# Kernel optimization log

Measured on AMD Instinct MI355X. Metric: run time of the kernel, lower is better.

The kernel has to match this reference:

```python
import jax, jax.numpy as jnp
import numpy as np
import math

HIDDEN = 768
HEADS = 12
HEAD_DIM = HIDDEN // HEADS  # 64
SEQ = 197
K_RANK = min(128, HEAD_DIM)  # 64
BATCH = 64


def setup_inputs() -> dict:
    key = jax.random.key(0)
    ks = jax.random.split(key, 12)
    init = 0.02
    # Linear weights stored [in, out] (equivalent to torch W.T)
    return {
        "hidden_states": jax.random.normal(ks[0], (BATCH, SEQ, HIDDEN), dtype=jnp.float32),
        "Wq": jax.random.normal(ks[1], (HIDDEN, HIDDEN), dtype=jnp.float32) * init,
        "bq": jnp.zeros((HIDDEN,), dtype=jnp.float32),
        "Wk": jax.random.normal(ks[2], (HIDDEN, HIDDEN), dtype=jnp.float32) * init,
        "bk": jnp.zeros((HIDDEN,), dtype=jnp.float32),
        "Wv": jax.random.normal(ks[3], (HIDDEN, HIDDEN), dtype=jnp.float32) * init,
        "bv": jnp.zeros((HIDDEN,), dtype=jnp.float32),
        "Wo": jax.random.normal(ks[4], (HIDDEN, HIDDEN), dtype=jnp.float32) * init,
        "bo": jnp.zeros((HIDDEN,), dtype=jnp.float32),
        "E_k": jax.random.normal(ks[5], (SEQ, K_RANK), dtype=jnp.float32) * init,
        "E_v": jax.random.normal(ks[6], (SEQ, K_RANK), dtype=jnp.float32) * init,
    }


def reference(hidden_states, Wq, bq, Wk, bk, Wv, bv, Wo, bo, E_k, E_v):
    B, S, D = hidden_states.shape
    H, d = HEADS, HEAD_DIM
    scale = 1.0 / math.sqrt(d)

    def split_heads(x):  # [B,S,D] -> [B,H,S,d]
        return x.reshape(B, S, H, d).transpose(0, 2, 1, 3)

    q = split_heads(hidden_states @ Wq + bq)
    k = split_heads(hidden_states @ Wk + bk)
    v = split_heads(hidden_states @ Wv + bv)

    # low-rank projection of K/V along the sequence axis: [B,H,k,d]
    pk = jnp.einsum('sk,bhsd->bhkd', E_k, k)
    pv = jnp.einsum('sk,bhsd->bhkd', E_v, v)

    # scores over reduced axis: [B,H,S,k]
    scores = jnp.einsum('bhsd,bhkd->bhsk', q, pk) * scale
    probs = jax.nn.softmax(scores, axis=-1)

    ctx = jnp.einsum('bhsk,bhkd->bhsd', probs, pv)
    ctx = ctx.transpose(0, 2, 1, 3).reshape(B, S, D)
    out = ctx @ Wo + bo  # dropout rate 0.0 -> identity
    return out
```

## Files before the change

### kernel.cpp

```cpp
#include <hip/hip_runtime.h>
#include <math.h>

#define B_   64
#define S_   197
#define D_   768
#define H_   12
#define HD_  64
#define M_   (B_ * S_)
#define MPAD 12672
#define KE   224
#define BH_  (B_ * H_)
#define WSZ  ((size_t)D_ * D_)

typedef _Float16 half8_t __attribute__((ext_vector_type(8)));
typedef _Float16 half4_t __attribute__((ext_vector_type(4)));
typedef _Float16 half2_t __attribute__((ext_vector_type(2)));
typedef float floatx4 __attribute__((ext_vector_type(4)));

#define LDS_DMA16(gptr, lptr) \
  __builtin_amdgcn_global_load_lds((const __attribute__((address_space(1))) void*)(gptr), \
                                   (__attribute__((address_space(3))) void*)(lptr), 16, 0, 0)

__global__ __launch_bounds__(256) void prep_y_kernel(
    const float* __restrict__ X,
    const float* __restrict__ Wq, const float* __restrict__ Wk,
    const float* __restrict__ Wv, const float* __restrict__ Wo,
    const float* __restrict__ Ek, const float* __restrict__ Ev,
    _Float16* __restrict__ Xh,
    _Float16* __restrict__ Tcat, _Float16* __restrict__ To,
    float* __restrict__ esumK, float* __restrict__ esumV,
    _Float16* __restrict__ Ybuf)
{
    __shared__ _Float16 smem[KE * 66];
    const int bid = blockIdx.x, tid = threadIdx.x;

    int task, idx;
    if (bid < 9984) {
        const int q = bid / 13, r = bid - q * 13;
        if (r == 0) { task = 0; idx = q; }
        else        { task = 1; idx = 12 * q + r - 1; }
    } else if (bid < 10272) { task = 1; idx = 9216 + (bid - 9984); }
    else if (bid < 12576)   { task = 2; idx = bid - 10272; }
    else                    { task = 3; idx = bid - 12576; }

    if (task == 1) {
        const int i4 = (idx * 256 + tid) * 4;
        float4 v = make_float4(0.f, 0.f, 0.f, 0.f);
        if (i4 < M_ * D_) v = *(const float4*)&X[i4];
        half4_t o = { (_Float16)v.x, (_Float16)v.y, (_Float16)v.z, (_Float16)v.w };
        *(half4_t*)&Xh[i4] = o;
        return;
    }

    if (task == 2) {
        float (*tile)[33] = (float (*)[33])smem;
        const int z = idx / 576, rem = idx % 576;
        const int bx = rem % 24, by = rem / 24;
        const float* W = (z == 0) ? Wk : (z == 1) ? Wv : (z == 2) ? Wq : Wo;
        _Float16* T = (z < 3) ? (Tcat + (size_t)z * WSZ) : To;
        const int n0 = bx * 32, k0 = by * 32;
        const int r = tid >> 3, c4 = (tid & 7) * 4;
        *(float4*)&tile[r][c4] = *(const float4*)&W[(size_t)(k0 + r) * D_ + n0 + c4];
        __syncthreads();
        half4_t o = { (_Float16)tile[c4 + 0][r], (_Float16)tile[c4 + 1][r],
                      (_Float16)tile[c4 + 2][r], (_Float16)tile[c4 + 3][r] };
        *(half4_t*)&T[(size_t)(n0 + r) * D_ + k0 + c4] = o;
        return;
    }

    if (task == 3) {
        const float* E = idx ? Ev : Ek;
        float* es = idx ? esumV : esumK;
        if (tid < 64) {
            float acc = 0.f;
            for (int s = 0; s < S_; ++s) acc += E[s * 64 + tid];
            es[tid] = acc;
        }
        return;
    }

    _Float16* Xs = smem;
    const int b = idx / 12, n0 = (idx % 12) * 64;
    const int w = tid >> 6, lane = tid & 63;
    const int l15 = lane & 15, quad = lane >> 4;

    #pragma unroll
    for (int i = 0; i < 7; ++i) {
        const int s = i * 32 + (tid >> 3);
        const int d0 = (tid & 7) * 8;
        float4 v0 = make_float4(0.f, 0.f, 0.f, 0.f), v1 = v0;
        if (s < S_) {
            const float* src = &X[(size_t)(b * S_ + s) * D_ + n0 + d0];
            v0 = *(const float4*)src;
            v1 = *(const float4*)(src + 4);
        }
        const _Float16 h[8] = { (_Float16)v0.x, (_Float16)v0.y, (_Float16)v0.z,
                                (_Float16)v0.w, (_Float16)v1.x, (_Float16)v1.y,
                                (_Float16)v1.z, (_Float16)v1.w };
        #pragma unroll
        for (int jj = 0; jj < 4; ++jj) {
            half2_t t2 = { h[2 * jj], h[2 * jj + 1] };
            *(half2_t*)&Xs[s * 66 + d0 + 2 * jj] = t2;
        }
    }
    __syncthreads();

    floatx4 acc[2][4] = {};
    #pragma unroll
    for (int k7 = 0; k7 < 7; ++k7) {
        half8_t af[2];
        #pragma unroll
        for (int mi = 0; mi < 2; ++mi) {
            const int row = w * 32 + mi * 16 + l15;
            const float* Esrc = (row < 64) ? Ek : Ev;
            const int er = row & 63;
            #pragma unroll
            for (int jj = 0; jj < 8; ++jj) {
                const int s = k7 * 32 + quad * 8 + jj;
                af[mi][jj] = (_Float16)((s < S_) ? Esrc[s * 64 + er] : 0.f);
            }
        }
        #pragma unroll
        for (int ni = 0; ni < 4; ++ni) {
            const int sb = k7 * 32 + quad * 8;
            half8_t bf;
            #pragma unroll
            for (int jj = 0; jj < 8; ++jj) bf[jj] = Xs[(sb + jj) * 66 + ni * 16 + l15];
            #pragma unroll
            for (int mi = 0; mi < 2; ++mi)
                acc[mi][ni] = __builtin_amdgcn_mfma_f32_16x16x32_f16(
                    af[mi], bf, acc[mi][ni], 0, 0, 0);
        }
    }

    #pragma unroll
    for (int mi = 0; mi < 2; ++mi)
        #pragma unroll
        for (int ni = 0; ni < 4; ++ni)
            #pragma unroll
            for (int i = 0; i < 4; ++i) {
                const int m_local = w * 32 + mi * 16 + quad * 4 + i;
                const int row = (m_local >> 6) * 4096 + b * 64 + (m_local & 63);
                Ybuf[(size_t)row * D_ + n0 + ni * 16 + l15] = (_Float16)acc[mi][ni][i];
            }
}

__global__ __launch_bounds__(256) void gemm_qpkv(
    const _Float16* __restrict__ Xh, const _Float16* __restrict__ Ybuf,
    const _Float16* __restrict__ Tcat,
    const float* __restrict__ bq, const float* __restrict__ bk,
    const float* __restrict__ bv,
    const float* __restrict__ esumK, const float* __restrict__ esumV,
    _Float16* __restrict__ Qh, _Float16* __restrict__ pk16,
    _Float16* __restrict__ pv16)
{
    __shared__ _Float16 sm[32768];
    const int bid = blockIdx.x;
    const _Float16 *A, *W;
    const float *bias, *esum;
    _Float16* O16;
    int m0, n0, rowb;
    if (bid < 624) {
        const int xcd = bid & 7, t = bid >> 3;
        const int slot = t / 6, j = t - slot * 6;
        const int m_blk = slot * 8 + xcd;
        if (m_blk >= MPAD / 128) return;
        m0 = m_blk * 128; n0 = j * 128; rowb = m0;
        A = Xh; W = Tcat + 2 * WSZ + (size_t)n0 * D_;
        bias = bq; esum = nullptr; O16 = Qh;
    } else {
        const int b2 = bid - 624;
        const int xcd = b2 & 7, t = b2 >> 3;
        const int slot = t / 6, j = t - slot * 6;
        const int m_blk = slot * 8 + xcd;
        m0 = m_blk * 128; n0 = j * 128;
        const bool pv = (m_blk >= 32);
        rowb = pv ? m0 - 4096 : m0;
        A = Ybuf; W = Tcat + (pv ? WSZ : 0) + (size_t)n0 * D_;
        bias = pv ? bv : bk; esum = pv ? esumV : esumK;
        O16 = pv ? pv16 : pk16;
    }

    const int tid = threadIdx.x;
    const int w = tid >> 6, lane = tid & 63;
    const int fr = lane & 15, quad = lane >> 4, f7 = lane & 7;
    const int l3 = lane >> 3;
    const int csrc = ((lane & 7) ^ l3) * 8;
    const int wm = (w >> 1) * 64, wn = (w & 1) * 64;

    const _Float16* Abase = A + (size_t)(m0 + w * 32 + l3) * D_ + csrc;
    const _Float16* Wbase = W + (size_t)(w * 32 + l3) * D_ + csrc;

    floatx4 acc[4][4] = {};

#define QPKV_STAGE(BUF, K0) \
    { _Pragma("unroll") \
      for (int j = 0; j < 4; ++j) { \
          LDS_DMA16(Abase + (size_t)(j * 8) * D_ + (K0), &sm[(BUF) * 16384 + w * 2048 + j * 512]); \
          LDS_DMA16(Wbase + (size_t)(j * 8) * D_ + (K0), &sm[(BUF) * 16384 + 8192 + w * 2048 + j * 512]); \
      } }

#define QPKV_COMPUTE(BUF) \
    { _Pragma("unroll") \
      for (int ksub = 0; ksub < 2; ++ksub) { \
          const int sa = ((ksub * 4 + quad) ^ f7) * 8; \
          half8_t af[4], bf[4]; \
          _Pragma("unroll") \
          for (int i = 0; i < 4; ++i) { \
              af[i] = *(const half8_t*)&sm[(BUF) * 16384 + (wm + i * 16 + fr) * 64 + sa]; \
              bf[i] = *(const half8_t*)&sm[(BUF) * 16384 + 8192 + (wn + i * 16 + fr) * 64 + sa]; \
          } \
          _Pragma("unroll") \
          for (int mi = 0; mi < 4; ++mi) \
              _Pragma("unroll") \
              for (int ni = 0; ni < 4; ++ni) \
                  acc[mi][ni] = __builtin_amdgcn_mfma_f32_16x16x32_f16( \
                      af[mi], bf[ni], acc[mi][ni], 0, 0, 0); \
      } }

    QPKV_STAGE(0, 0);
    __syncthreads();
    #pragma unroll
    for (int t = 0; t < 10; t += 2) {
        QPKV_STAGE(1, (t + 1) * 64);
        QPKV_COMPUTE(0);
        __syncthreads();
        QPKV_STAGE(0, (t + 2) * 64);
        QPKV_COMPUTE(1);
        __syncthreads();
    }
    QPKV_STAGE(1, 11 * 64);
    QPKV_COMPUTE(0);
    __syncthreads();
    QPKV_COMPUTE(1);

    float bval[4];
    #pragma unroll
    for (int ni = 0; ni < 4; ++ni)
        bval[ni] = bias[n0 + wn + ni * 16 + fr];

    _Float16* ct = &sm[w * 2176];
    #pragma unroll
    for (int half = 0; half < 2; ++half) {
        #pragma unroll
        for (int mi2 = 0; mi2 < 2; ++mi2) {
            const int mi = half * 2 + mi2;
            float esv[4] = {1.f, 1.f, 1.f, 1.f};
            if (esum) {
                const float4 es4 = *(const float4*)&esum[mi * 16 + quad * 4];
                esv[0] = es4.x; esv[1] = es4.y; esv[2] = es4.z; esv[3] = es4.w;
            }
            #pragma unroll
            for (int ni = 0; ni < 4; ++ni)
                #pragma unroll
                for (int i = 0; i < 4; ++i)
                    ct[(mi2 * 16 + quad * 4 + i) * 68 + ni * 16 + fr] =
                        (_Float16)(acc[mi][ni][i] + esv[i] * bval[ni]);
        }
        #pragma unroll
        for (int pass = 0; pass < 4; ++pass) {
            const int rr = pass * 8 + (lane >> 3);
            const int cc = (lane & 7) * 8;
            const half8_t v = *(const half8_t*)&ct[rr * 68 + cc];
            *(half8_t*)&O16[(size_t)(rowb + wm + half * 32 + rr) * D_ + n0 + wn + cc] = v;
        }
    }
}

__global__ __launch_bounds__(256) void gemm_o(
    const _Float16* __restrict__ CTX, const _Float16* __restrict__ To,
    const float* __restrict__ bo, float* __restrict__ O32)
{
    __shared__ _Float16 sm[32768];
    const int xcd = blockIdx.x & 7, t = blockIdx.x >> 3;
    const int slot = t / 6, j = t - slot * 6;
    const int m_blk = slot * 8 + xcd;
    if (m_blk >= MPAD / 128) return;
    const int m0 = m_blk * 128, n0 = j * 128;

    const int tid = threadIdx.x;
    const int w = tid >> 6, lane = tid & 63;
    const int fr = lane & 15, quad = lane >> 4, f7 = lane & 7;
    const int l3 = lane >> 3;
    const int csrc = ((lane & 7) ^ l3) * 8;
    const int wm = (w >> 1) * 64, wn = (w & 1) * 64;

    const _Float16* Abase = CTX + (size_t)(m0 + w * 32 + l3) * D_ + csrc;
    const _Float16* Wbase = To + (size_t)(n0 + w * 32 + l3) * D_ + csrc;

    floatx4 acc[4][4] = {};

    QPKV_STAGE(0, 0);
    __syncthreads();
    #pragma unroll
    for (int t2 = 0; t2 < 10; t2 += 2) {
        QPKV_STAGE(1, (t2 + 1) * 64);
        QPKV_COMPUTE(0);
        __syncthreads();
        QPKV_STAGE(0, (t2 + 2) * 64);
        QPKV_COMPUTE(1);
        __syncthreads();
    }
    QPKV_STAGE(1, 11 * 64);
    QPKV_COMPUTE(0);
    __syncthreads();
    QPKV_COMPUTE(1);

    float bval[4];
    #pragma unroll
    for (int ni = 0; ni < 4; ++ni)
        bval[ni] = bo[n0 + wn + ni * 16 + fr];

    const bool full = (m0 + 128 <= M_);
    #pragma unroll
    for (int ni = 0; ni < 4; ++ni) {
        const int n = n0 + wn + ni * 16 + fr;
        #pragma unroll
        for (int mi = 0; mi < 4; ++mi)
            #pragma unroll
            for (int i = 0; i < 4; ++i) {
                const int m = m0 + wm + mi * 16 + quad * 4 + i;
                if (full || m < M_)
                    O32[(size_t)m * D_ + n] = acc[mi][ni][i] + bval[ni];
            }
    }
}

__global__ __launch_bounds__(256) void attn_kernel(
    const _Float16* __restrict__ Qh, const _Float16* __restrict__ pk16,
    const _Float16* __restrict__ pv16, _Float16* __restrict__ CTXh)
{
    __shared__ _Float16 P[64 * 80];
    const int bh = blockIdx.x, b = bh / H_, h = bh % H_;
    const int tid = threadIdx.x, w = tid >> 6, lane = tid & 63;
    const int l15 = lane & 15, quad = lane >> 4;
    const _Float16* pkB = pk16 + (size_t)(b * 64) * D_ + h * 64;
    const _Float16* pvB = pv16 + (size_t)(b * 64) * D_ + h * 64;
    const size_t qbase = (size_t)(b * S_) * D_ + h * HD_;

    half8_t bkf[4][2], bvf[4][2];
    #pragma unroll
    for (int ni = 0; ni < 4; ++ni)
        #pragma unroll
        for (int kk = 0; kk < 2; ++kk) {
            bkf[ni][kk] = *(const half8_t*)&pkB[(size_t)(ni * 16 + l15) * D_ + kk * 32 + quad * 8];
            #pragma unroll
            for (int jj = 0; jj < 8; ++jj)
                bvf[ni][kk][jj] = pvB[(size_t)(kk * 32 + quad * 8 + jj) * D_ + ni * 16 + l15];
        }

    for (int t = w; t < 13; t += 4) {
        const int srow = t * 16;
        floatx4 acc[4] = {};
        #pragma unroll
        for (int kk = 0; kk < 2; ++kk) {
            const half8_t aq = *(const half8_t*)
                &Qh[qbase + (size_t)(srow + l15) * D_ + kk * 32 + quad * 8];
            #pragma unroll
            for (int ni = 0; ni < 4; ++ni)
                acc[ni] = __builtin_amdgcn_mfma_f32_16x16x32_f16(
                    aq, bkf[ni][kk], acc[ni], 0, 0, 0);
        }
        float p[4][4];
        #pragma unroll
        for (int i = 0; i < 4; ++i) {
            const float s0 = acc[0][i] * 0.125f, s1 = acc[1][i] * 0.125f;
            const float s2 = acc[2][i] * 0.125f, s3 = acc[3][i] * 0.125f;
            float mx = fmaxf(fmaxf(s0, s1), fmaxf(s2, s3));
            #pragma unroll
            for (int off = 1; off < 16; off <<= 1)
                mx = fmaxf(mx, __shfl_xor(mx, off, 64));
            const float e0 = __expf(s0 - mx), e1 = __expf(s1 - mx);
            const float e2 = __expf(s2 - mx), e3 = __expf(s3 - mx);
            float sme = e0 + e1 + e2 + e3;
            #pragma unroll
            for (int off = 1; off < 16; off <<= 1)
                sme += __shfl_xor(sme, off, 64);
            const float inv = 1.f / sme;
            p[0][i] = e0 * inv; p[1][i] = e1 * inv;
            p[2][i] = e2 * inv; p[3][i] = e3 * inv;
        }
        #pragma unroll
        for (int ni = 0; ni < 4; ++ni)
            #pragma unroll
            for (int i = 0; i < 4; ++i)
                P[(w * 16 + quad * 4 + i) * 80 + ni * 16 + l15] = (_Float16)p[ni][i];

        floatx4 accv[4] = {};
        #pragma unroll
        for (int kk = 0; kk < 2; ++kk) {
            const half8_t ap = *(const half8_t*)&P[(w * 16 + l15) * 80 + kk * 32 + quad * 8];
            #pragma unroll
            for (int ni = 0; ni < 4; ++ni)
                accv[ni] = __builtin_amdgcn_mfma_f32_16x16x32_f16(
                    ap, bvf[ni][kk], accv[ni], 0, 0, 0);
        }
        #pragma unroll
        for (int ni = 0; ni < 4; ++ni)
            #pragma unroll
            for (int i = 0; i < 4; ++i) {
                const int s = srow + quad * 4 + i;
                if (s < S_)
                    CTXh[qbase + (size_t)s * D_ + ni * 16 + l15] = (_Float16)accv[ni][i];
            }
    }
}

extern "C" void kernel_launch(void* const* d_in, const int* in_sizes, int n_in,
                              void* d_out, int out_size, void* d_ws, size_t ws_size,
                              hipStream_t stream) {
    const float* X   = (const float*)d_in[0];
    const float* Wq  = (const float*)d_in[1];
    const float* bq  = (const float*)d_in[2];
    const float* Wk  = (const float*)d_in[3];
    const float* bk  = (const float*)d_in[4];
    const float* Wv  = (const float*)d_in[5];
    const float* bv  = (const float*)d_in[6];
    const float* Wo  = (const float*)d_in[7];
    const float* bo  = (const float*)d_in[8];
    const float* E_k = (const float*)d_in[9];
    const float* E_v = (const float*)d_in[10];
    float* out = (float*)d_out;

    char* p = (char*)d_ws;
    _Float16* Xh   = (_Float16*)p; p += (size_t)MPAD * D_ * 2;
    _Float16* Tcat = (_Float16*)p; p += (size_t)3 * WSZ * 2;
    _Float16* To   = (_Float16*)p; p += (size_t)WSZ * 2;
    _Float16* Qh   = (_Float16*)p; p += (size_t)MPAD * D_ * 2;
    float* esumK   = (float*)p;    p += 64 * sizeof(float);
    float* esumV   = (float*)p;    p += 64 * sizeof(float);
    _Float16* Ybuf = (_Float16*)p; p += (size_t)8192 * D_ * 2;
    _Float16* pk16 = (_Float16*)p; p += (size_t)4096 * D_ * 2;
    _Float16* pv16 = (_Float16*)p;

    prep_y_kernel<<<12578, 256, 0, stream>>>(X, Wq, Wk, Wv, Wo, E_k, E_v,
                                             Xh, Tcat, To, esumK, esumV, Ybuf);
    gemm_qpkv<<<1008, 256, 0, stream>>>(Xh, Ybuf, Tcat,
                                        bq, bk, bv, esumK, esumV,
                                        Qh, pk16, pv16);
    attn_kernel<<<BH_, 256, 0, stream>>>(Qh, pk16, pv16, Xh);
    gemm_o<<<624, 256, 0, stream>>>(Xh, To, bo, out);
}
```

Before: 202.0 us.

## Fuse fp32-to-fp16 conversion of X into the Q projection GEMM A-load

Drops the separate pass that converts the whole hidden_states tensor to fp16 in the prep kernel. The Q GEMM now reads fp32 X directly into registers, converts it and writes it to LDS, replacing the async LDS DMA path for the A operand. This removes one full write and read of an fp16 copy of X. The cost is register-staged loads with bounds checks and reads of twice as many bytes per A tile, which may weaken load/compute overlap in the Q blocks.

```diff
diff --git a/kernel.cpp b/kernel.cpp
--- a/kernel.cpp
+++ b/kernel.cpp
@@ -26,7 +26,6 @@
     const float* __restrict__ Wq, const float* __restrict__ Wk,
     const float* __restrict__ Wv, const float* __restrict__ Wo,
     const float* __restrict__ Ek, const float* __restrict__ Ev,
-    _Float16* __restrict__ Xh,
     _Float16* __restrict__ Tcat, _Float16* __restrict__ To,
     float* __restrict__ esumK, float* __restrict__ esumV,
     _Float16* __restrict__ Ybuf)
@@ -34,25 +33,8 @@
     __shared__ _Float16 smem[KE * 66];
     const int bid = blockIdx.x, tid = threadIdx.x;
 
-    int task, idx;
-    if (bid < 9984) {
-        const int q = bid / 13, r = bid - q * 13;
-        if (r == 0) { task = 0; idx = q; }
-        else        { task = 1; idx = 12 * q + r - 1; }
-    } else if (bid < 10272) { task = 1; idx = 9216 + (bid - 9984); }
-    else if (bid < 12576)   { task = 2; idx = bid - 10272; }
-    else                    { task = 3; idx = bid - 12576; }
-
-    if (task == 1) {
-        const int i4 = (idx * 256 + tid) * 4;
-        float4 v = make_float4(0.f, 0.f, 0.f, 0.f);
-        if (i4 < M_ * D_) v = *(const float4*)&X[i4];
-        half4_t o = { (_Float16)v.x, (_Float16)v.y, (_Float16)v.z, (_Float16)v.w };
-        *(half4_t*)&Xh[i4] = o;
-        return;
-    }
-
-    if (task == 2) {
+    if (bid >= 768 && bid < 3072) {
+        const int idx = bid - 768;
         float (*tile)[33] = (float (*)[33])smem;
         const int z = idx / 576, rem = idx % 576;
         const int bx = rem % 24, by = rem / 24;
@@ -68,7 +50,8 @@
         return;
     }
 
-    if (task == 3) {
+    if (bid >= 3072) {
+        const int idx = bid - 3072;
         const float* E = idx ? Ev : Ek;
         float* es = idx ? esumV : esumK;
         if (tid < 64) {
@@ -80,6 +63,7 @@
     }
 
     _Float16* Xs = smem;
+    const int idx = bid;
     const int b = idx / 12, n0 = (idx % 12) * 64;
     const int w = tid >> 6, lane = tid & 63;
     const int l15 = lane & 15, quad = lane >> 4;
@@ -146,7 +130,7 @@
 }
 
 __global__ __launch_bounds__(256) void gemm_qpkv(
-    const _Float16* __restrict__ Xh, const _Float16* __restrict__ Ybuf,
+    const float* __restrict__ X, const _Float16* __restrict__ Ybuf,
     const _Float16* __restrict__ Tcat,
     const float* __restrict__ bq, const float* __restrict__ bk,
     const float* __restrict__ bv,
@@ -156,18 +140,19 @@
 {
     __shared__ _Float16 sm[32768];
     const int bid = blockIdx.x;
-    const _Float16 *A, *W;
+    const _Float16 *W;
     const float *bias, *esum;
     _Float16* O16;
     int m0, n0, rowb;
+    bool isQ;
     if (bid < 624) {
         const int xcd = bid & 7, t = bid >> 3;
         const int slot = t / 6, j = t - slot * 6;
         const int m_blk = slot * 8 + xcd;
         if (m_blk >= MPAD / 128) return;
         m0 = m_blk * 128; n0 = j * 128; rowb = m0;
-        A = Xh; W = Tcat + 2 * WSZ + (size_t)n0 * D_;
-        bias = bq; esum = nullptr; O16 = Qh;
+        W = Tcat + 2 * WSZ + (size_t)n0 * D_;
+        bias = bq; esum = nullptr; O16 = Qh; isQ = true;
     } else {
         const int b2 = bid - 624;
         const int xcd = b2 & 7, t = b2 >> 3;
@@ -176,9 +161,9 @@
         m0 = m_blk * 128; n0 = j * 128;
         const bool pv = (m_blk >= 32);
         rowb = pv ? m0 - 4096 : m0;
-        A = Ybuf; W = Tcat + (pv ? WSZ : 0) + (size_t)n0 * D_;
+        W = Tcat + (pv ? WSZ : 0) + (size_t)n0 * D_;
         bias = pv ? bv : bk; esum = pv ? esumV : esumK;
-        O16 = pv ? pv16 : pk16;
+        O16 = pv ? pv16 : pk16; isQ = false;
     }
 
     const int tid = threadIdx.x;
@@ -188,19 +173,15 @@
     const int csrc = ((lane & 7) ^ l3) * 8;
     const int wm = (w >> 1) * 64, wn = (w & 1) * 64;
 
-    const _Float16* Abase = A + (size_t)(m0 + w * 32 + l3) * D_ + csrc;
     const _Float16* Wbase = W + (size_t)(w * 32 + l3) * D_ + csrc;
-
     floatx4 acc[4][4] = {};
 
-#define QPKV_STAGE(BUF, K0) \
+#define STAGE_B(BUF, K0) \
     { _Pragma("unroll") \
-      for (int j = 0; j < 4; ++j) { \
-          LDS_DMA16(Abase + (size_t)(j * 8) * D_ + (K0), &sm[(BUF) * 16384 + w * 2048 + j * 512]); \
-          LDS_DMA16(Wbase + (size_t)(j * 8) * D_ + (K0), &sm[(BUF) * 16384 + 8192 + w * 2048 + j * 512]); \
-      } }
-
-#define QPKV_COMPUTE(BUF) \
+      for (int j = 0; j < 4; ++j) \
+          LDS_DMA16(Wbase + (size_t)(j * 8) * D_ + (K0), &sm[(BUF) * 16384 + 8192 + w * 2048 + j * 512]); }
+
+#define COMPUTE(BUF) \
     { _Pragma("unroll") \
       for (int ksub = 0; ksub < 2; ++ksub) { \
           const int sa = ((ksub * 4 + quad) ^ f7) * 8; \
@@ -218,21 +199,73 @@
                       af[mi], bf[ni], acc[mi][ni], 0, 0, 0); \
       } }
 
-    QPKV_STAGE(0, 0);
-    __syncthreads();
-    #pragma unroll
-    for (int t = 0; t < 10; t += 2) {
-        QPKV_STAGE(1, (t + 1) * 64);
-        QPKV_COMPUTE(0);
-        __syncthreads();
-        QPKV_STAGE(0, (t + 2) * 64);
-        QPKV_COMPUTE(1);
-        __syncthreads();
-    }
-    QPKV_STAGE(1, 11 * 64);
-    QPKV_COMPUTE(0);
-    __syncthreads();
-    QPKV_COMPUTE(1);
+    if (isQ) {
+        const float* Xbase = X + (size_t)(m0 + w * 32 + l3) * D_ + csrc;
+        float4 ra[4][2];
+        const float4 z4 = make_float4(0.f, 0.f, 0.f, 0.f);
+
+#define LOADA(K0) \
+        { _Pragma("unroll") \
+          for (int j = 0; j < 4; ++j) { \
+              const int r = m0 + w * 32 + j * 8 + l3; \
+              if (r < M_) { \
+                  ra[j][0] = *(const float4*)(Xbase + (size_t)(j * 8) * D_ + (K0)); \
+                  ra[j][1] = *(const float4*)(Xbase + (size_t)(j * 8) * D_ + (K0) + 4); \
+              } else { ra[j][0] = z4; ra[j][1] = z4; } \
+          } }
+
+#define WRITE_A(BUF) \
+        { _Pragma("unroll") \
+          for (int j = 0; j < 4; ++j) { \
+              half8_t o = { (_Float16)ra[j][0].x, (_Float16)ra[j][0].y, \
+                            (_Float16)ra[j][0].z, (_Float16)ra[j][0].w, \
+                            (_Float16)ra[j][1].x, (_Float16)ra[j][1].y, \
+                            (_Float16)ra[j][1].z, (_Float16)ra[j][1].w }; \
+              *(half8_t*)&sm[(BUF) * 16384 + w * 2048 + j * 512 + lane * 8] = o; \
+          } }
+
+        LOADA(0); STAGE_B(0, 0); WRITE_A(0);
+        __syncthreads();
+        #pragma unroll
+        for (int t = 0; t < 10; t += 2) {
+            LOADA((t + 1) * 64); STAGE_B(1, (t + 1) * 64);
+            COMPUTE(0);
+            WRITE_A(1);
+            __syncthreads();
+            LOADA((t + 2) * 64); STAGE_B(0, (t + 2) * 64);
+            COMPUTE(1);
+            WRITE_A(0);
+            __syncthreads();
+        }
+        LOADA(11 * 64); STAGE_B(1, 11 * 64);
+        COMPUTE(0);
+        WRITE_A(1);
+        __syncthreads();
+        COMPUTE(1);
+    } else {
+        const _Float16* Abase = Ybuf + (size_t)(m0 + w * 32 + l3) * D_ + csrc;
+
+#define STAGE_A16(BUF, K0) \
+        { _Pragma("unroll") \
+          for (int j = 0; j < 4; ++j) \
+              LDS_DMA16(Abase + (size_t)(j * 8) * D_ + (K0), &sm[(BUF) * 16384 + w * 2048 + j * 512]); }
+
+        STAGE_A16(0, 0); STAGE_B(0, 0);
+        __syncthreads();
+        #pragma unroll
+        for (int t = 0; t < 10; t += 2) {
+            STAGE_A16(1, (t + 1) * 64); STAGE_B(1, (t + 1) * 64);
+            COMPUTE(0);
+            __syncthreads();
+            STAGE_A16(0, (t + 2) * 64); STAGE_B(0, (t + 2) * 64);
+            COMPUTE(1);
+            __syncthreads();
+        }
+        STAGE_A16(1, 11 * 64); STAGE_B(1, 11 * 64);
+        COMPUTE(0);
+        __syncthreads();
+        COMPUTE(1);
+    }
 
     float bval[4];
     #pragma unroll
@@ -290,21 +323,28 @@
 
     floatx4 acc[4][4] = {};
 
-    QPKV_STAGE(0, 0);
+#define O_STAGE(BUF, K0) \
+    { _Pragma("unroll") \
+      for (int j2 = 0; j2 < 4; ++j2) { \
+          LDS_DMA16(Abase + (size_t)(j2 * 8) * D_ + (K0), &sm[(BUF) * 16384 + w * 2048 + j2 * 512]); \
+          LDS_DMA16(Wbase + (size_t)(j2 * 8) * D_ + (K0), &sm[(BUF) * 16384 + 8192 + w * 2048 + j2 * 512]); \
+      } }
+
+    O_STAGE(0, 0);
     __syncthreads();
     #pragma unroll
     for (int t2 = 0; t2 < 10; t2 += 2) {
-        QPKV_STAGE(1, (t2 + 1) * 64);
-        QPKV_COMPUTE(0);
-        __syncthreads();
-        QPKV_STAGE(0, (t2 + 2) * 64);
-        QPKV_COMPUTE(1);
-        __syncthreads();
-    }
-    QPKV_STAGE(1, 11 * 64);
-    QPKV_COMPUTE(0);
+        O_STAGE(1, (t2 + 1) * 64);
+        COMPUTE(0);
+        __syncthreads();
+        O_STAGE(0, (t2 + 2) * 64);
+        COMPUTE(1);
+        __syncthreads();
+    }
+    O_STAGE(1, 11 * 64);
+    COMPUTE(0);
     __syncthreads();
-    QPKV_COMPUTE(1);
+    COMPUTE(1);
 
     float bval[4];
     #pragma unroll
@@ -423,7 +463,7 @@
     float* out = (float*)d_out;
 
     char* p = (char*)d_ws;
-    _Float16* Xh   = (_Float16*)p; p += (size_t)MPAD * D_ * 2;
+    _Float16* CTXh = (_Float16*)p; p += (size_t)MPAD * D_ * 2;
     _Float16* Tcat = (_Float16*)p; p += (size_t)3 * WSZ * 2;
     _Float16* To   = (_Float16*)p; p += (size_t)WSZ * 2;
     _Float16* Qh   = (_Float16*)p; p += (size_t)MPAD * D_ * 2;
@@ -433,11 +473,11 @@
     _Float16* pk16 = (_Float16*)p; p += (size_t)4096 * D_ * 2;
     _Float16* pv16 = (_Float16*)p;
 
-    prep_y_kernel<<<12578, 256, 0, stream>>>(X, Wq, Wk, Wv, Wo, E_k, E_v,
-                                             Xh, Tcat, To, esumK, esumV, Ybuf);
-    gemm_qpkv<<<1008, 256, 0, stream>>>(Xh, Ybuf, Tcat,
+    prep_y_kernel<<<3074, 256, 0, stream>>>(X, Wq, Wk, Wv, Wo, E_k, E_v,
+                                            Tcat, To, esumK, esumV, Ybuf);
+    gemm_qpkv<<<1008, 256, 0, stream>>>(X, Ybuf, Tcat,
                                         bq, bk, bv, esumK, esumV,
                                         Qh, pk16, pv16);
-    attn_kernel<<<BH_, 256, 0, stream>>>(Qh, pk16, pv16, Xh);
-    gemm_o<<<624, 256, 0, stream>>>(Xh, To, bo, out);
+    attn_kernel<<<BH_, 256, 0, stream>>>(Qh, pk16, pv16, CTXh);
+    gemm_o<<<624, 256, 0, stream>>>(CTXh, To, bo, out);
 }
```

After: 220.0 us. 1.09x slower.

## Fuse attention and output projection into a single kernel

Applied to the files above, without the earlier changes.

Replaces the separate attention kernel and the output-projection GEMM with one kernel. Each block handles 32 sequence rows of one batch across all 12 heads, one wave per 3 heads, and keeps the context tile in LDS. It then multiplies that tile by the Wo weights, read directly from global memory, and writes the fp32 output with bias. This removes the fp16 context round trip through global memory and one kernel launch. In exchange, Wo is re-read by every block with little register reuse and no LDS staging, and far fewer blocks run than the tiled GEMM used.

```diff
diff --git a/kernel.cpp b/kernel.cpp
--- a/kernel.cpp
+++ b/kernel.cpp
@@ -11,6 +11,7 @@
 #define KE   224
 #define BH_  (B_ * H_)
 #define WSZ  ((size_t)D_ * D_)
+#define CW   776
 
 typedef _Float16 half8_t __attribute__((ext_vector_type(8)));
 typedef _Float16 half4_t __attribute__((ext_vector_type(4)));
@@ -267,141 +268,142 @@
     }
 }
 
-__global__ __launch_bounds__(256) void gemm_o(
-    const _Float16* __restrict__ CTX, const _Float16* __restrict__ To,
+__global__ __launch_bounds__(256) void attn_o_kernel(
+    const _Float16* __restrict__ Qh, const _Float16* __restrict__ pk16,
+    const _Float16* __restrict__ pv16, const _Float16* __restrict__ To,
     const float* __restrict__ bo, float* __restrict__ O32)
 {
-    __shared__ _Float16 sm[32768];
-    const int xcd = blockIdx.x & 7, t = blockIdx.x >> 3;
-    const int slot = t / 6, j = t - slot * 6;
-    const int m_blk = slot * 8 + xcd;
-    if (m_blk >= MPAD / 128) return;
-    const int m0 = m_blk * 128, n0 = j * 128;
-
-    const int tid = threadIdx.x;
-    const int w = tid >> 6, lane = tid & 63;
-    const int fr = lane & 15, quad = lane >> 4, f7 = lane & 7;
-    const int l3 = lane >> 3;
-    const int csrc = ((lane & 7) ^ l3) * 8;
-    const int wm = (w >> 1) * 64, wn = (w & 1) * 64;
-
-    const _Float16* Abase = CTX + (size_t)(m0 + w * 32 + l3) * D_ + csrc;
-    const _Float16* Wbase = To + (size_t)(n0 + w * 32 + l3) * D_ + csrc;
-
-    floatx4 acc[4][4] = {};
-
-    QPKV_STAGE(0, 0);
-    __syncthreads();
-    #pragma unroll
-    for (int t2 = 0; t2 < 10; t2 += 2) {
-        QPKV_STAGE(1, (t2 + 1) * 64);
-        QPKV_COMPUTE(0);
-        __syncthreads();
-        QPKV_STAGE(0, (t2 + 2) * 64);
-        QPKV_COMPUTE(1);
-        __syncthreads();
-    }
-    QPKV_STAGE(1, 11 * 64);
-    QPKV_COMPUTE(0);
-    __syncthreads();
-    QPKV_COMPUTE(1);
-
-    float bval[4];
-    #pragma unroll
-    for (int ni = 0; ni < 4; ++ni)
-        bval[ni] = bo[n0 + wn + ni * 16 + fr];
-
-    const bool full = (m0 + 128 <= M_);
-    #pragma unroll
-    for (int ni = 0; ni < 4; ++ni) {
-        const int n = n0 + wn + ni * 16 + fr;
-        #pragma unroll
-        for (int mi = 0; mi < 4; ++mi)
-            #pragma unroll
-            for (int i = 0; i < 4; ++i) {
-                const int m = m0 + wm + mi * 16 + quad * 4 + i;
-                if (full || m < M_)
-                    O32[(size_t)m * D_ + n] = acc[mi][ni][i] + bval[ni];
-            }
-    }
-}
-
-__global__ __launch_bounds__(256) void attn_kernel(
-    const _Float16* __restrict__ Qh, const _Float16* __restrict__ pk16,
-    const _Float16* __restrict__ pv16, _Float16* __restrict__ CTXh)
-{
-    __shared__ _Float16 P[64 * 80];
-    const int bh = blockIdx.x, b = bh / H_, h = bh % H_;
+    __shared__ _Float16 ctx[32 * CW];
+    const int bid = blockIdx.x;
+    const int b = bid & 63, st = bid >> 6;
+    const int srow0 = st * 32;
     const int tid = threadIdx.x, w = tid >> 6, lane = tid & 63;
     const int l15 = lane & 15, quad = lane >> 4;
-    const _Float16* pkB = pk16 + (size_t)(b * 64) * D_ + h * 64;
-    const _Float16* pvB = pv16 + (size_t)(b * 64) * D_ + h * 64;
-    const size_t qbase = (size_t)(b * S_) * D_ + h * HD_;
-
-    half8_t bkf[4][2], bvf[4][2];
-    #pragma unroll
-    for (int ni = 0; ni < 4; ++ni)
+
+    _Float16* P = &ctx[(w * 3 + 2) * 64];
+
+    for (int hh = 0; hh < 3; ++hh) {
+        const int h = w * 3 + hh;
+        const _Float16* pkB = pk16 + (size_t)(b * 64) * D_ + h * 64;
+        const _Float16* pvB = pv16 + (size_t)(b * 64) * D_ + h * 64;
+        const size_t qbase = (size_t)(b * S_) * D_ + h * HD_;
+
+        half8_t bkf[4][2], bvf[4][2];
+        #pragma unroll
+        for (int ni = 0; ni < 4; ++ni)
+            #pragma unroll
+            for (int kk = 0; kk < 2; ++kk) {
+                bkf[ni][kk] = *(const half8_t*)&pkB[(size_t)(ni * 16 + l15) * D_ + kk * 32 + quad * 8];
+                #pragma unroll
+                for (int jj = 0; jj < 8; ++jj)
+                    bvf[ni][kk][jj] = pvB[(size_t)(kk * 32 + quad * 8 + jj) * D_ + ni * 16 + l15];
+            }
+
+        floatx4 acc[2][4] = {};
         #pragma unroll
         for (int kk = 0; kk < 2; ++kk) {
-            bkf[ni][kk] = *(const half8_t*)&pkB[(size_t)(ni * 16 + l15) * D_ + kk * 32 + quad * 8];
-            #pragma unroll
-            for (int jj = 0; jj < 8; ++jj)
-                bvf[ni][kk][jj] = pvB[(size_t)(kk * 32 + quad * 8 + jj) * D_ + ni * 16 + l15];
-        }
-
-    for (int t = w; t < 13; t += 4) {
-        const int srow = t * 16;
-        floatx4 acc[4] = {};
+            half8_t aq[2];
+            #pragma unroll
+            for (int mi = 0; mi < 2; ++mi)
+                aq[mi] = *(const half8_t*)
+                    &Qh[qbase + (size_t)(srow0 + mi * 16 + l15) * D_ + kk * 32 + quad * 8];
+            #pragma unroll
+            for (int ni = 0; ni < 4; ++ni)
+                #pragma unroll
+                for (int mi = 0; mi < 2; ++mi)
+                    acc[mi][ni] = __builtin_amdgcn_mfma_f32_16x16x32_f16(
+                        aq[mi], bkf[ni][kk], acc[mi][ni], 0, 0, 0);
+        }
+
+        #pragma unroll
+        for (int mi = 0; mi < 2; ++mi) {
+            float p[4][4];
+            #pragma unroll
+            for (int i = 0; i < 4; ++i) {
+                const float s0 = acc[mi][0][i] * 0.125f, s1 = acc[mi][1][i] * 0.125f;
+                const float s2 = acc[mi][2][i] * 0.125f, s3 = acc[mi][3][i] * 0.125f;
+                float mx = fmaxf(fmaxf(s0, s1), fmaxf(s2, s3));
+                #pragma unroll
+                for (int off = 1; off < 16; off <<= 1)
+                    mx = fmaxf(mx, __shfl_xor(mx, off, 64));
+                const float e0 = __expf(s0 - mx), e1 = __expf(s1 - mx);
+                const float e2 = __expf(s2 - mx), e3 = __expf(s3 - mx);
+                float sme = e0 + e1 + e2 + e3;
+                #pragma unroll
+                for (int off = 1; off < 16; off <<= 1)
+                    sme += __shfl_xor(sme, off, 64);
+                const float inv = 1.f / sme;
+                p[0][i] = e0 * inv; p[1][i] = e1 * inv;
+                p[2][i] = e2 * inv; p[3][i] = e3 * inv;
+            }
+            #pragma unroll
+            for (int ni = 0; ni < 4; ++ni)
+                #pragma unroll
+                for (int i = 0; i < 4; ++i)
+                    P[(mi * 16 + quad * 4 + i) * CW + ni * 16 + l15] = (_Float16)p[ni][i];
+        }
+
+        floatx4 accv[2][4] = {};
         #pragma unroll
         for (int kk = 0; kk < 2; ++kk) {
-            const half8_t aq = *(const half8_t*)
-                &Qh[qbase + (size_t)(srow + l15) * D_ + kk * 32 + quad * 8];
+            half8_t ap[2];
+            #pragma unroll
+            for (int mi = 0; mi < 2; ++mi)
+                ap[mi] = *(const half8_t*)&P[(mi * 16 + l15) * CW + kk * 32 + quad * 8];
             #pragma unroll
             for (int ni = 0; ni < 4; ++ni)
-                acc[ni] = __builtin_amdgcn_mfma_f32_16x16x32_f16(
-                    aq, bkf[ni][kk], acc[ni], 0, 0, 0);
-        }
-        float p[4][4];
-        #pragma unroll
-        for (int i = 0; i < 4; ++i) {
-            const float s0 = acc[0][i] * 0.125f, s1 = acc[1][i] * 0.125f;
-            const float s2 = acc[2][i] * 0.125f, s3 = acc[3][i] * 0.125f;
-            float mx = fmaxf(fmaxf(s0, s1), fmaxf(s2, s3));
-            #pragma unroll
-            for (int off = 1; off < 16; off <<= 1)
-                mx = fmaxf(mx, __shfl_xor(mx, off, 64));
-            const float e0 = __expf(s0 - mx), e1 = __expf(s1 - mx);
-            const float e2 = __expf(s2 - mx), e3 = __expf(s3 - mx);
-            float sme = e0 + e1 + e2 + e3;
-            #pragma unroll
-            for (int off = 1; off < 16; off <<= 1)
-                sme += __shfl_xor(sme, off, 64);
-            const float inv = 1.f / sme;
-            p[0][i] = e0 * inv; p[1][i] = e1 * inv;
-            p[2][i] = e2 * inv; p[3][i] = e3 * inv;
-        }
-        #pragma unroll
-        for (int ni = 0; ni < 4; ++ni)
-            #pragma unroll
-            for (int i = 0; i < 4; ++i)
-                P[(w * 16 + quad * 4 + i) * 80 + ni * 16 + l15] = (_Float16)p[ni][i];
-
-        floatx4 accv[4] = {};
-        #pragma unroll
-        for (int kk = 0; kk < 2; ++kk) {
-            const half8_t ap = *(const half8_t*)&P[(w * 16 + l15) * 80 + kk * 32 + quad * 8];
+                #pragma unroll
+                for (int mi = 0; mi < 2; ++mi)
+                    accv[mi][ni] = __builtin_amdgcn_mfma_f32_16x16x32_f16(
+                        ap[mi], bvf[ni][kk], accv[mi][ni], 0, 0, 0);
+        }
+        #pragma unroll
+        for (int mi = 0; mi < 2; ++mi)
             #pragma unroll
             for (int ni = 0; ni < 4; ++ni)
-                accv[ni] = __builtin_amdgcn_mfma_f32_16x16x32_f16(
-                    ap, bvf[ni][kk], accv[ni], 0, 0, 0);
-        }
-        #pragma unroll
-        for (int ni = 0; ni < 4; ++ni)
+                #pragma unroll
+                for (int i = 0; i < 4; ++i)
+                    ctx[(mi * 16 + quad * 4 + i) * CW + h * 64 + ni * 16 + l15] =
+                        (_Float16)accv[mi][ni][i];
+    }
+    __syncthreads();
+
+    float bval[12];
+    #pragma unroll
+    for (int nf = 0; nf < 12; ++nf)
+        bval[nf] = bo[w * 192 + nf * 16 + l15];
+
+    floatx4 oacc[2][12] = {};
+    for (int k0 = 0; k0 < 12; ++k0) {
+        #pragma unroll
+        for (int ksub = 0; ksub < 2; ++ksub) {
+            const int ka = k0 * 64 + ksub * 32 + quad * 8;
+            half8_t af[2];
+            #pragma unroll
+            for (int mi = 0; mi < 2; ++mi)
+                af[mi] = *(const half8_t*)&ctx[(mi * 16 + l15) * CW + ka];
+            #pragma unroll
+            for (int nf = 0; nf < 12; ++nf) {
+                const half8_t bf = *(const half8_t*)
+                    &To[(size_t)(w * 192 + nf * 16 + l15) * D_ + ka];
+                #pragma unroll
+                for (int mi = 0; mi < 2; ++mi)
+                    oacc[mi][nf] = __builtin_amdgcn_mfma_f32_16x16x32_f16(
+                        af[mi], bf, oacc[mi][nf], 0, 0, 0);
+            }
+        }
+    }
+
+    #pragma unroll
+    for (int nf = 0; nf < 12; ++nf) {
+        const int n = w * 192 + nf * 16 + l15;
+        #pragma unroll
+        for (int mi = 0; mi < 2; ++mi)
             #pragma unroll
             for (int i = 0; i < 4; ++i) {
-                const int s = srow + quad * 4 + i;
+                const int s = srow0 + mi * 16 + quad * 4 + i;
                 if (s < S_)
-                    CTXh[qbase + (size_t)s * D_ + ni * 16 + l15] = (_Float16)accv[ni][i];
+                    O32[(size_t)(b * S_ + s) * D_ + n] = oacc[mi][nf][i] + bval[nf];
             }
     }
 }
@@ -438,6 +440,5 @@
     gemm_qpkv<<<1008, 256, 0, stream>>>(Xh, Ybuf, Tcat,
                                         bq, bk, bv, esumK, esumV,
                                         Qh, pk16, pv16);
-    attn_kernel<<<BH_, 256, 0, stream>>>(Qh, pk16, pv16, Xh);
-    gemm_o<<<624, 256, 0, stream>>>(Xh, To, bo, out);
+    attn_o_kernel<<<448, 256, 0, stream>>>(Qh, pk16, pv16, To, bo, out);
 }
```

New measurement: 292.3 us. 44.7% more time.

## Fuse X fp16 conversion into Y-projection blocks and store projected V transposed

Applied to the files above, without the earlier changes.

The separate elementwise blocks that converted X to fp16 are removed; each Y-projection block already reads its X tile, so it now also writes the fp16 copy to Xh, and a few small blocks zero the padded tail rows. This avoids reading X from global memory twice and shrinks the prep grid. In addition, the projected V is written transposed ([D][4096]) through LDS in the GEMM epilogue, so the attention kernel can load V fragments with one 16-byte vector load instead of eight strided scalar loads. The cost is an extra LDS transpose pass in the GEMM epilogue.

```diff
diff --git a/kernel.cpp b/kernel.cpp
--- a/kernel.cpp
+++ b/kernel.cpp
@@ -34,25 +34,8 @@
     __shared__ _Float16 smem[KE * 66];
     const int bid = blockIdx.x, tid = threadIdx.x;
 
-    int task, idx;
-    if (bid < 9984) {
-        const int q = bid / 13, r = bid - q * 13;
-        if (r == 0) { task = 0; idx = q; }
-        else        { task = 1; idx = 12 * q + r - 1; }
-    } else if (bid < 10272) { task = 1; idx = 9216 + (bid - 9984); }
-    else if (bid < 12576)   { task = 2; idx = bid - 10272; }
-    else                    { task = 3; idx = bid - 12576; }
-
-    if (task == 1) {
-        const int i4 = (idx * 256 + tid) * 4;
-        float4 v = make_float4(0.f, 0.f, 0.f, 0.f);
-        if (i4 < M_ * D_) v = *(const float4*)&X[i4];
-        half4_t o = { (_Float16)v.x, (_Float16)v.y, (_Float16)v.z, (_Float16)v.w };
-        *(half4_t*)&Xh[i4] = o;
-        return;
-    }
-
-    if (task == 2) {
+    if (bid >= 768 && bid < 3072) {
+        const int idx = bid - 768;
         float (*tile)[33] = (float (*)[33])smem;
         const int z = idx / 576, rem = idx % 576;
         const int bx = rem % 24, by = rem / 24;
@@ -68,7 +51,8 @@
         return;
     }
 
-    if (task == 3) {
+    if (bid >= 3096) {
+        const int idx = bid - 3096;
         const float* E = idx ? Ev : Ek;
         float* es = idx ? esumV : esumK;
         if (tid < 64) {
@@ -79,7 +63,15 @@
         return;
     }
 
+    if (bid >= 3072) {
+        const int idx = bid - 3072;
+        const half8_t z8 = {};
+        *(half8_t*)&Xh[(size_t)M_ * D_ + (size_t)(idx * 256 + tid) * 8] = z8;
+        return;
+    }
+
     _Float16* Xs = smem;
+    const int idx = bid;
     const int b = idx / 12, n0 = (idx % 12) * 64;
     const int w = tid >> 6, lane = tid & 63;
     const int l15 = lane & 15, quad = lane >> 4;
@@ -94,12 +86,14 @@
             v0 = *(const float4*)src;
             v1 = *(const float4*)(src + 4);
         }
-        const _Float16 h[8] = { (_Float16)v0.x, (_Float16)v0.y, (_Float16)v0.z,
-                                (_Float16)v0.w, (_Float16)v1.x, (_Float16)v1.y,
-                                (_Float16)v1.z, (_Float16)v1.w };
+        const half8_t h8 = { (_Float16)v0.x, (_Float16)v0.y, (_Float16)v0.z,
+                             (_Float16)v0.w, (_Float16)v1.x, (_Float16)v1.y,
+                             (_Float16)v1.z, (_Float16)v1.w };
+        if (s < S_)
+            *(half8_t*)&Xh[(size_t)(b * S_ + s) * D_ + n0 + d0] = h8;
         #pragma unroll
         for (int jj = 0; jj < 4; ++jj) {
-            half2_t t2 = { h[2 * jj], h[2 * jj + 1] };
+            half2_t t2 = { h8[2 * jj], h8[2 * jj + 1] };
             *(half2_t*)&Xs[s * 66 + d0 + 2 * jj] = t2;
         }
     }
@@ -152,7 +146,7 @@
     const float* __restrict__ bv,
     const float* __restrict__ esumK, const float* __restrict__ esumV,
     _Float16* __restrict__ Qh, _Float16* __restrict__ pk16,
-    _Float16* __restrict__ pv16)
+    _Float16* __restrict__ pvT)
 {
     __shared__ _Float16 sm[32768];
     const int bid = blockIdx.x;
@@ -160,6 +154,7 @@
     const float *bias, *esum;
     _Float16* O16;
     int m0, n0, rowb;
+    bool pvt = false;
     if (bid < 624) {
         const int xcd = bid & 7, t = bid >> 3;
         const int slot = t / 6, j = t - slot * 6;
@@ -175,10 +170,11 @@
         const int m_blk = slot * 8 + xcd;
         m0 = m_blk * 128; n0 = j * 128;
         const bool pv = (m_blk >= 32);
+        pvt = pv;
         rowb = pv ? m0 - 4096 : m0;
         A = Ybuf; W = Tcat + (pv ? WSZ : 0) + (size_t)n0 * D_;
         bias = pv ? bv : bk; esum = pv ? esumV : esumK;
-        O16 = pv ? pv16 : pk16;
+        O16 = pk16;
     }
 
     const int tid = threadIdx.x;
@@ -240,6 +236,35 @@
         bval[ni] = bias[n0 + wn + ni * 16 + fr];
 
     _Float16* ct = &sm[w * 2176];
+
+    if (pvt) {
+        #pragma unroll
+        for (int half = 0; half < 2; ++half) {
+            #pragma unroll
+            for (int ni2 = 0; ni2 < 2; ++ni2) {
+                const int ni = half * 2 + ni2;
+                #pragma unroll
+                for (int mi = 0; mi < 4; ++mi) {
+                    const float4 es4 = *(const float4*)&esum[mi * 16 + quad * 4];
+                    const float esv[4] = { es4.x, es4.y, es4.z, es4.w };
+                    #pragma unroll
+                    for (int i = 0; i < 4; ++i)
+                        ct[(ni2 * 16 + fr) * 68 + mi * 16 + quad * 4 + i] =
+                            (_Float16)(acc[mi][ni][i] + esv[i] * bval[ni]);
+                }
+            }
+            #pragma unroll
+            for (int pass = 0; pass < 4; ++pass) {
+                const int rr = pass * 8 + (lane >> 3);
+                const int cc = (lane & 7) * 8;
+                const half8_t v = *(const half8_t*)&ct[rr * 68 + cc];
+                *(half8_t*)&pvT[(size_t)(n0 + wn + half * 32 + rr) * 4096
+                                + rowb + wm + cc] = v;
+            }
+        }
+        return;
+    }
+
     #pragma unroll
     for (int half = 0; half < 2; ++half) {
         #pragma unroll
@@ -328,14 +353,14 @@
 
 __global__ __launch_bounds__(256) void attn_kernel(
     const _Float16* __restrict__ Qh, const _Float16* __restrict__ pk16,
-    const _Float16* __restrict__ pv16, _Float16* __restrict__ CTXh)
+    const _Float16* __restrict__ pvT, _Float16* __restrict__ CTXh)
 {
     __shared__ _Float16 P[64 * 80];
     const int bh = blockIdx.x, b = bh / H_, h = bh % H_;
     const int tid = threadIdx.x, w = tid >> 6, lane = tid & 63;
     const int l15 = lane & 15, quad = lane >> 4;
     const _Float16* pkB = pk16 + (size_t)(b * 64) * D_ + h * 64;
-    const _Float16* pvB = pv16 + (size_t)(b * 64) * D_ + h * 64;
+    const _Float16* pvB = pvT + (size_t)(h * 64) * 4096 + b * 64;
     const size_t qbase = (size_t)(b * S_) * D_ + h * HD_;
 
     half8_t bkf[4][2], bvf[4][2];
@@ -344,9 +369,7 @@
         #pragma unroll
         for (int kk = 0; kk < 2; ++kk) {
             bkf[ni][kk] = *(const half8_t*)&pkB[(size_t)(ni * 16 + l15) * D_ + kk * 32 + quad * 8];
-            #pragma unroll
-            for (int jj = 0; jj < 8; ++jj)
-                bvf[ni][kk][jj] = pvB[(size_t)(kk * 32 + quad * 8 + jj) * D_ + ni * 16 + l15];
+            bvf[ni][kk] = *(const half8_t*)&pvB[(size_t)(ni * 16 + l15) * 4096 + kk * 32 + quad * 8];
         }
 
     for (int t = w; t < 13; t += 4) {
@@ -431,13 +454,13 @@
     float* esumV   = (float*)p;    p += 64 * sizeof(float);
     _Float16* Ybuf = (_Float16*)p; p += (size_t)8192 * D_ * 2;
     _Float16* pk16 = (_Float16*)p; p += (size_t)4096 * D_ * 2;
-    _Float16* pv16 = (_Float16*)p;
-
-    prep_y_kernel<<<12578, 256, 0, stream>>>(X, Wq, Wk, Wv, Wo, E_k, E_v,
-                                             Xh, Tcat, To, esumK, esumV, Ybuf);
+    _Float16* pvT  = (_Float16*)p;
+
+    prep_y_kernel<<<3098, 256, 0, stream>>>(X, Wq, Wk, Wv, Wo, E_k, E_v,
+                                            Xh, Tcat, To, esumK, esumV, Ybuf);
     gemm_qpkv<<<1008, 256, 0, stream>>>(Xh, Ybuf, Tcat,
                                         bq, bk, bv, esumK, esumV,
-                                        Qh, pk16, pv16);
-    attn_kernel<<<BH_, 256, 0, stream>>>(Qh, pk16, pv16, Xh);
+                                        Qh, pk16, pvT);
+    attn_kernel<<<BH_, 256, 0, stream>>>(Qh, pk16, pvT, Xh);
     gemm_o<<<624, 256, 0, stream>>>(Xh, To, bo, out);
 }
```

Measured after the change: 196.5 us. 1.03x faster.
